# Kernel optimization log

Hardware: AMD Instinct MI355X
Metric: run time of the kernel (lower is better)

## Reference

```python
import jax, jax.numpy as jnp
import numpy as np

N_NODES = 50000
N_EDGES = 800000
IN_FEAT = 512
OUT_FEAT = 128


def multispike(x):
    return jnp.floor(jnp.clip(4.0 * x, 0.0, 4.0) + 0.5) / 4.0


def setup_inputs() -> dict:
    key = jax.random.key(0)
    k1, k2, k3, k4, k5 = jax.random.split(key, 5)
    feat = jax.random.normal(k1, (N_NODES, IN_FEAT), dtype=jnp.float32)
    # Xavier-uniform-like init for the weight parameter
    limit = np.sqrt(6.0 / (IN_FEAT + OUT_FEAT)).astype(np.float32)
    weight = jax.random.uniform(k2, (IN_FEAT, OUT_FEAT), dtype=jnp.float32,
                                minval=-limit, maxval=limit)
    rows = jnp.sort(jax.random.randint(k3, (N_EDGES,), 0, N_NODES, dtype=jnp.int32))
    cols = jax.random.randint(k4, (N_EDGES,), 0, N_NODES, dtype=jnp.int32)
    edge_weight = jax.random.uniform(k5, (N_EDGES,), dtype=jnp.float32)
    return {"feat": feat, "weight": weight, "rows": rows, "cols": cols,
            "edge_weight": edge_weight}


def reference(feat, weight, rows, cols, edge_weight):
    # x = feat @ W                     [N, out_feat]
    x = jnp.matmul(feat, weight)
    # x = spmm(adj, x): out[i] = sum_{e: rows[e]==i} w_e * x[cols[e]]
    edge_feats = edge_weight[:, None] * x[cols]          # [E, out_feat]
    x = jax.ops.segment_sum(edge_feats, rows, num_segments=N_NODES)
    # quantized multi-spike activation
    return multispike(x)
```

## Files before the change

### kernel.cpp

```cpp
#include <hip/hip_runtime.h>

#define N_NODES 50000
#define N_EDGES 800000
#define IN_FEAT 512
#define OUT_FEAT 128


__device__ __forceinline__ float multispike(float a) {
    return floorf(fminf(fmaxf(4.0f * a, 0.0f), 4.0f) + 0.5f) * 0.25f;
}

__device__ __forceinline__ int bswz(int q) { return q ^ ((q >> 3) & 1); }

__global__ __launch_bounds__(128) void gemm_kernel(const float* __restrict__ A,
                                                   const float* __restrict__ B,
                                                   float* __restrict__ C, int M) {
    __shared__ float As[32][68];
    __shared__ float Bs[32][128];

    const int tid = threadIdx.x;
    const int tx = tid & 15;
    const int ty = tid >> 4;
    const int block_m = blockIdx.x * 64;

    const int bq0 = bswz(2 * tx) * 4;
    const int bq1 = bswz(2 * tx + 1) * 4;

    float acc[8][8];
#pragma unroll
    for (int i = 0; i < 8; i++)
#pragma unroll
        for (int j = 0; j < 8; j++) acc[i][j] = 0.0f;

    for (int k0 = 0; k0 < IN_FEAT; k0 += 32) {
#pragma unroll
        for (int i = 0; i < 4; i++) {
            int f = tid + i * 128;
            int r = f >> 3;
            int kq = (f & 7) << 2;
            int gm = block_m + r;
            float4 v = make_float4(0.f, 0.f, 0.f, 0.f);
            if (gm < M) v = *(const float4*)(A + (size_t)gm * IN_FEAT + k0 + kq);
            As[kq + 0][r] = v.x;
            As[kq + 1][r] = v.y;
            As[kq + 2][r] = v.z;
            As[kq + 3][r] = v.w;
        }
#pragma unroll
        for (int i = 0; i < 8; i++) {
            int f = tid + i * 128;
            int r = f >> 5;
            int q = f & 31;
            *(float4*)&Bs[r][bswz(q) * 4] =
                *(const float4*)(B + (size_t)(k0 + r) * OUT_FEAT + q * 4);
        }
        __syncthreads();

#pragma unroll
        for (int k = 0; k < 32; k++) {
            float4 a0 = *(const float4*)&As[k][ty * 8];
            float4 a1 = *(const float4*)&As[k][ty * 8 + 4];
            float4 b0 = *(const float4*)&Bs[k][bq0];
            float4 b1 = *(const float4*)&Bs[k][bq1];
            float av[8] = {a0.x, a0.y, a0.z, a0.w, a1.x, a1.y, a1.z, a1.w};
            float bv[8] = {b0.x, b0.y, b0.z, b0.w, b1.x, b1.y, b1.z, b1.w};
#pragma unroll
            for (int i = 0; i < 8; i++)
#pragma unroll
                for (int j = 0; j < 8; j++)
                    acc[i][j] = fmaf(av[i], bv[j], acc[i][j]);
        }
        __syncthreads();
    }

#pragma unroll
    for (int i = 0; i < 8; i++) {
        int gm = block_m + ty * 8 + i;
        if (gm < M) {
            float* cp = C + (size_t)gm * OUT_FEAT + tx * 8;
            *(float4*)cp = make_float4(acc[i][0], acc[i][1], acc[i][2], acc[i][3]);
            *(float4*)(cp + 4) = make_float4(acc[i][4], acc[i][5], acc[i][6], acc[i][7]);
        }
    }
}

__global__ __launch_bounds__(256) void rowptr_kernel(const int* __restrict__ rows,
                                                     int* __restrict__ row_ptr) {
    int i = blockIdx.x * blockDim.x + threadIdx.x;
    if (i > N_NODES) return;
    int lo = 0, hi = N_EDGES;
    while (lo < hi) {
        int mid = (lo + hi) >> 1;
        if (rows[mid] < i) lo = mid + 1; else hi = mid;
    }
    row_ptr[i] = lo;
}

__global__ __launch_bounds__(256) void spmm_kernel(const float* __restrict__ x,
                                                   const int* __restrict__ cols,
                                                   const float* __restrict__ ew,
                                                   const int* __restrict__ row_ptr,
                                                   float* __restrict__ out) {
    const int wave = threadIdx.x >> 6;
    const int lane = threadIdx.x & 63;
    const int r = blockIdx.x * 4 + wave;
    if (r >= N_NODES) return;

    const int e0 = row_ptr[r];
    const int e1 = row_ptr[r + 1];
    const float2* __restrict__ x2 = (const float2*)x;

    float accx = 0.0f, accy = 0.0f;
    int e = e0;
    for (; e + 8 <= e1; e += 8) {
        int c[8];
        float w[8];
        float2 v[8];
#pragma unroll
        for (int j = 0; j < 8; j++) {
            c[j] = cols[e + j];
            w[j] = ew[e + j];
        }
#pragma unroll
        for (int j = 0; j < 8; j++) {
            v[j] = x2[(size_t)c[j] * 64 + lane];
        }
#pragma unroll
        for (int j = 0; j < 8; j++) {
            accx = fmaf(w[j], v[j].x, accx);
            accy = fmaf(w[j], v[j].y, accy);
        }
    }
    for (; e < e1; e++) {
        int c = cols[e];
        float w = ew[e];
        float2 v = x2[(size_t)c * 64 + lane];
        accx = fmaf(w, v.x, accx);
        accy = fmaf(w, v.y, accy);
    }
    float2* out2 = (float2*)out;
    out2[(size_t)r * 64 + lane] = make_float2(multispike(accx), multispike(accy));
}

extern "C" void kernel_launch(void* const* d_in, const int* in_sizes, int n_in,
                              void* d_out, int out_size, void* d_ws, size_t ws_size,
                              hipStream_t stream) {
    const float* feat = (const float*)d_in[0];
    const float* weight = (const float*)d_in[1];
    const int* rows = (const int*)d_in[2];
    const int* cols = (const int*)d_in[3];
    const float* ew = (const float*)d_in[4];
    float* out = (float*)d_out;

    float* x = (float*)d_ws;
    int* row_ptr = (int*)((char*)d_ws + (size_t)N_NODES * OUT_FEAT * sizeof(float));

    rowptr_kernel<<<(N_NODES + 256) / 256, 256, 0, stream>>>(rows, row_ptr);
    gemm_kernel<<<(N_NODES + 63) / 64, 128, 0, stream>>>(feat, weight, x, N_NODES);
    spmm_kernel<<<(N_NODES + 3) / 4, 256, 0, stream>>>(x, cols, ew, row_ptr, out);
}
```

Before: 317.9 us.

## Prefetch next GEMM k-tile into registers while computing current tile

The GEMM now loads the next 32-wide k-slice of A and B into registers (48 extra VGPRs) right after the shared-memory barrier, then runs the FMA loop on the current tile. A sched_barrier keeps the compiler from sinking those global loads past the compute loop. The goal is to hide global-memory latency behind the FMAs. The cost is higher register pressure on top of the 64 accumulators, which may lower occupancy.

```diff
diff --git a/kernel.cpp b/kernel.cpp
--- a/kernel.cpp
+++ b/kernel.cpp
@@ -32,29 +32,66 @@
 #pragma unroll
         for (int j = 0; j < 8; j++) acc[i][j] = 0.0f;
 
-    for (int k0 = 0; k0 < IN_FEAT; k0 += 32) {
+    float4 av[4];
+    float4 bv[8];
+
+#pragma unroll
+    for (int i = 0; i < 4; i++) {
+        int f = tid + i * 128;
+        int r = f >> 3;
+        int kq = (f & 7) << 2;
+        int gm = block_m + r;
+        av[i] = make_float4(0.f, 0.f, 0.f, 0.f);
+        if (gm < M) av[i] = *(const float4*)(A + (size_t)gm * IN_FEAT + kq);
+    }
+#pragma unroll
+    for (int i = 0; i < 8; i++) {
+        int f = tid + i * 128;
+        int r = f >> 5;
+        int q = f & 31;
+        bv[i] = *(const float4*)(B + (size_t)r * OUT_FEAT + q * 4);
+    }
+
+    for (int t = 0; t < 16; t++) {
 #pragma unroll
         for (int i = 0; i < 4; i++) {
             int f = tid + i * 128;
             int r = f >> 3;
             int kq = (f & 7) << 2;
-            int gm = block_m + r;
-            float4 v = make_float4(0.f, 0.f, 0.f, 0.f);
-            if (gm < M) v = *(const float4*)(A + (size_t)gm * IN_FEAT + k0 + kq);
-            As[kq + 0][r] = v.x;
-            As[kq + 1][r] = v.y;
-            As[kq + 2][r] = v.z;
-            As[kq + 3][r] = v.w;
+            As[kq + 0][r] = av[i].x;
+            As[kq + 1][r] = av[i].y;
+            As[kq + 2][r] = av[i].z;
+            As[kq + 3][r] = av[i].w;
         }
 #pragma unroll
         for (int i = 0; i < 8; i++) {
             int f = tid + i * 128;
             int r = f >> 5;
             int q = f & 31;
-            *(float4*)&Bs[r][bswz(q) * 4] =
-                *(const float4*)(B + (size_t)(k0 + r) * OUT_FEAT + q * 4);
+            *(float4*)&Bs[r][bswz(q) * 4] = bv[i];
         }
         __syncthreads();
+
+        if (t < 15) {
+            const int k0 = (t + 1) * 32;
+#pragma unroll
+            for (int i = 0; i < 4; i++) {
+                int f = tid + i * 128;
+                int r = f >> 3;
+                int kq = (f & 7) << 2;
+                int gm = block_m + r;
+                av[i] = make_float4(0.f, 0.f, 0.f, 0.f);
+                if (gm < M) av[i] = *(const float4*)(A + (size_t)gm * IN_FEAT + k0 + kq);
+            }
+#pragma unroll
+            for (int i = 0; i < 8; i++) {
+                int f = tid + i * 128;
+                int r = f >> 5;
+                int q = f & 31;
+                bv[i] = *(const float4*)(B + (size_t)(k0 + r) * OUT_FEAT + q * 4);
+            }
+            __builtin_amdgcn_sched_barrier(0);
+        }
 
 #pragma unroll
         for (int k = 0; k < 32; k++) {
@@ -62,13 +99,13 @@
             float4 a1 = *(const float4*)&As[k][ty * 8 + 4];
             float4 b0 = *(const float4*)&Bs[k][bq0];
             float4 b1 = *(const float4*)&Bs[k][bq1];
-            float av[8] = {a0.x, a0.y, a0.z, a0.w, a1.x, a1.y, a1.z, a1.w};
-            float bv[8] = {b0.x, b0.y, b0.z, b0.w, b1.x, b1.y, b1.z, b1.w};
+            float avv[8] = {a0.x, a0.y, a0.z, a0.w, a1.x, a1.y, a1.z, a1.w};
+            float bvv[8] = {b0.x, b0.y, b0.z, b0.w, b1.x, b1.y, b1.z, b1.w};
 #pragma unroll
             for (int i = 0; i < 8; i++)
 #pragma unroll
                 for (int j = 0; j < 8; j++)
-                    acc[i][j] = fmaf(av[i], bv[j], acc[i][j]);
+                    acc[i][j] = fmaf(avv[i], bvv[j], acc[i][j]);
         }
         __syncthreads();
     }
```

Result: slower. 357.2 us (+12.4%).

## Double-buffer B via direct global-to-LDS loads and read A straight from global

Applied to the files above, without the earlier changes.

The GEMM stops staging A in shared memory; each thread reads its own 8 rows of A directly from global memory as float4 and prefetches the first chunk of the next k-tile. B is double-buffered in LDS and filled with global_load_lds, so the next tile's copy overlaps compute and the transposed A scatter into shared memory is gone. Launch bounds request two blocks per CU. The risk is extra global and L1 traffic for A, since the 16 threads sharing a row each reload it, and higher register pressure from the prefetch buffers.

```diff
diff --git a/kernel.cpp b/kernel.cpp
--- a/kernel.cpp
+++ b/kernel.cpp
@@ -12,11 +12,10 @@
 
 __device__ __forceinline__ int bswz(int q) { return q ^ ((q >> 3) & 1); }
 
-__global__ __launch_bounds__(128) void gemm_kernel(const float* __restrict__ A,
-                                                   const float* __restrict__ B,
-                                                   float* __restrict__ C, int M) {
-    __shared__ float As[32][68];
-    __shared__ float Bs[32][128];
+__global__ __launch_bounds__(128, 2) void gemm_kernel(const float* __restrict__ A,
+                                                      const float* __restrict__ B,
+                                                      float* __restrict__ C, int M) {
+    __shared__ float Bs[2][32][128];
 
     const int tid = threadIdx.x;
     const int tx = tid & 15;
@@ -26,49 +25,82 @@
     const int bq0 = bswz(2 * tx) * 4;
     const int bq1 = bswz(2 * tx + 1) * 4;
 
+    const float* arow[8];
+#pragma unroll
+    for (int i = 0; i < 8; i++) {
+        int gm = block_m + ty * 8 + i;
+        arow[i] = A + (size_t)(gm < M ? gm : 0) * IN_FEAT;
+    }
+
     float acc[8][8];
 #pragma unroll
     for (int i = 0; i < 8; i++)
 #pragma unroll
         for (int j = 0; j < 8; j++) acc[i][j] = 0.0f;
 
-    for (int k0 = 0; k0 < IN_FEAT; k0 += 32) {
-#pragma unroll
-        for (int i = 0; i < 4; i++) {
-            int f = tid + i * 128;
-            int r = f >> 3;
-            int kq = (f & 7) << 2;
-            int gm = block_m + r;
-            float4 v = make_float4(0.f, 0.f, 0.f, 0.f);
-            if (gm < M) v = *(const float4*)(A + (size_t)gm * IN_FEAT + k0 + kq);
-            As[kq + 0][r] = v.x;
-            As[kq + 1][r] = v.y;
-            As[kq + 2][r] = v.z;
-            As[kq + 3][r] = v.w;
-        }
+    auto stage = [&](int buf, int k0) {
 #pragma unroll
         for (int i = 0; i < 8; i++) {
-            int f = tid + i * 128;
-            int r = f >> 5;
-            int q = f & 31;
-            *(float4*)&Bs[r][bswz(q) * 4] =
-                *(const float4*)(B + (size_t)(k0 + r) * OUT_FEAT + q * 4);
+            int s = tid + i * 128;
+            int r = s >> 5;
+            int p = s & 31;
+            const float* src = B + (size_t)(k0 + r) * OUT_FEAT + bswz(p) * 4;
+            float* dst = &Bs[buf][0][0] + (size_t)s * 4;
+            __builtin_amdgcn_global_load_lds(
+                (const __attribute__((address_space(1))) void*)src,
+                (__attribute__((address_space(3))) void*)dst, 16, 0, 0);
         }
-        __syncthreads();
+    };
+
+    stage(0, 0);
+    float4 an[8];
+#pragma unroll
+    for (int i = 0; i < 8; i++) an[i] = *(const float4*)(arow[i]);
+    __syncthreads();
+
+    for (int t = 0; t < 16; t++) {
+        const int k0 = t * 32;
+        const int cur = t & 1;
+
+        if (t < 15) stage(cur ^ 1, k0 + 32);
+
+        float4 a0[8];
+#pragma unroll
+        for (int i = 0; i < 8; i++) a0[i] = an[i];
+        if (t < 15) {
+#pragma unroll
+            for (int i = 0; i < 8; i++)
+                an[i] = *(const float4*)(arow[i] + k0 + 32);
+        }
 
 #pragma unroll
-        for (int k = 0; k < 32; k++) {
-            float4 a0 = *(const float4*)&As[k][ty * 8];
-            float4 a1 = *(const float4*)&As[k][ty * 8 + 4];
-            float4 b0 = *(const float4*)&Bs[k][bq0];
-            float4 b1 = *(const float4*)&Bs[k][bq1];
-            float av[8] = {a0.x, a0.y, a0.z, a0.w, a1.x, a1.y, a1.z, a1.w};
-            float bv[8] = {b0.x, b0.y, b0.z, b0.w, b1.x, b1.y, b1.z, b1.w};
+        for (int kq = 0; kq < 8; kq++) {
+            float4 a[8];
+            if (kq == 0) {
 #pragma unroll
-            for (int i = 0; i < 8; i++)
+                for (int i = 0; i < 8; i++) a[i] = a0[i];
+            } else {
 #pragma unroll
-                for (int j = 0; j < 8; j++)
-                    acc[i][j] = fmaf(av[i], bv[j], acc[i][j]);
+                for (int i = 0; i < 8; i++)
+                    a[i] = *(const float4*)(arow[i] + k0 + kq * 4);
+            }
+#pragma unroll
+            for (int kk = 0; kk < 4; kk++) {
+                const int k = kq * 4 + kk;
+                float4 b0 = *(const float4*)&Bs[cur][k][bq0];
+                float4 b1 = *(const float4*)&Bs[cur][k][bq1];
+                float bvv[8] = {b0.x, b0.y, b0.z, b0.w, b1.x, b1.y, b1.z, b1.w};
+                float avv[8];
+#pragma unroll
+                for (int i = 0; i < 8; i++)
+                    avv[i] = (kk == 0) ? a[i].x : (kk == 1) ? a[i].y
+                           : (kk == 2) ? a[i].z : a[i].w;
+#pragma unroll
+                for (int i = 0; i < 8; i++)
+#pragma unroll
+                    for (int j = 0; j < 8; j++)
+                        acc[i][j] = fmaf(avv[i], bvv[j], acc[i][j]);
+            }
         }
         __syncthreads();
     }
```

After: 404.2 us. 1.27x slower.
